# Kernel tuning notes

Hardware: AMD Instinct MI355X
Metric: run time of the kernel (lower is better)

## Reference

```python
import jax, jax.numpy as jnp
import numpy as np

B, S, H, NH, HD = 2, 2048, 4096, 32, 128
THETA = 10000.0


def rotate_half(x):
    x1, x2 = jnp.split(x, 2, axis=-1)
    return jnp.concatenate((-x2, x1), axis=-1)


def setup_inputs() -> dict:
    key = jax.random.key(0)
    ks = jax.random.split(key, 6)
    hidden_states = jax.random.normal(ks[0], (B, S, H), dtype=jnp.float32)
    # additive causal mask, [1,1,S,S]
    causal = jnp.triu(jnp.full((S, S), -1e9, dtype=jnp.float32), k=1)
    attention_mask = causal[None, None, :, :]
    scale = 0.02
    Wq = jax.random.normal(ks[1], (H, H), dtype=jnp.float32) * scale
    Wk = jax.random.normal(ks[2], (H, H), dtype=jnp.float32) * scale
    Wv = jax.random.normal(ks[3], (H, H), dtype=jnp.float32) * scale
    Wo = jax.random.normal(ks[4], (H, H), dtype=jnp.float32) * scale
    return {"hidden_states": hidden_states, "attention_mask": attention_mask,
            "Wq": Wq, "Wk": Wk, "Wv": Wv, "Wo": Wo}


def _rope_tables(seq_len, dtype):
    inv_freq = 1.0 / (THETA ** (jnp.arange(0, HD, 2, dtype=jnp.float32) / HD))
    t = jnp.arange(seq_len, dtype=jnp.float32)
    freqs = jnp.einsum('i,j->ij', t, inv_freq)          # [S, HD/2]
    emb = jnp.concatenate((freqs, freqs), axis=-1)       # [S, HD]
    return jnp.cos(emb).astype(dtype), jnp.sin(emb).astype(dtype)


def reference(hidden_states, attention_mask, Wq, Wk, Wv, Wo):
    b, s, _ = hidden_states.shape
    # nn.Linear: y = x @ W.T
    q = jnp.einsum('bsh,oh->bso', hidden_states, Wq).reshape(b, s, NH, HD).transpose(0, 2, 1, 3)
    k = jnp.einsum('bsh,oh->bso', hidden_states, Wk).reshape(b, s, NH, HD).transpose(0, 2, 1, 3)
    v = jnp.einsum('bsh,oh->bso', hidden_states, Wv).reshape(b, s, NH, HD).transpose(0, 2, 1, 3)
    cos, sin = _rope_tables(s, q.dtype)                  # [S, HD] broadcast over b,h
    q = q * cos + rotate_half(q) * sin
    k = k * cos + rotate_half(k) * sin
    scores = jnp.einsum('bhqd,bhkd->bhqk', q, k) / jnp.sqrt(jnp.asarray(HD, q.dtype))
    scores = scores + attention_mask
    attn = jax.nn.softmax(scores.astype(jnp.float32), axis=-1).astype(q.dtype)
    out = jnp.einsum('bhqk,bhkd->bhqd', attn, v)
    out = out.transpose(0, 2, 1, 3).reshape(b, s, H)
    return jnp.einsum('bsh,oh->bso', out, Wo)
```

## Files before the change

### kernel.cpp

```cpp
#include <hip/hip_runtime.h>
#include <stdint.h>

typedef __attribute__((ext_vector_type(4))) float f32x4;
typedef __attribute__((ext_vector_type(8))) short bf16x8;
typedef __attribute__((ext_vector_type(4))) unsigned int u32x4;

__device__ __forceinline__ short f2bf(float x) {
  unsigned int u = __builtin_bit_cast(unsigned int, x);
  unsigned int r = (u + 0x7fffu + ((u >> 16) & 1u)) >> 16;
  return (short)r;
}
__device__ __forceinline__ float bf2f(short s) {
  unsigned int u = ((unsigned int)(unsigned short)s) << 16;
  return __builtin_bit_cast(float, u);
}
__device__ __forceinline__ unsigned pkbf(float lo, float hi) {
  unsigned r;
  asm("v_cvt_pk_bf16_f32 %0, %1, %2" : "=v"(r) : "v"(lo), "v"(hi));
  return r;
}

__device__ __forceinline__ void gload_lds16(const void* g, void* l) {
  __builtin_amdgcn_global_load_lds(
      (const __attribute__((address_space(1))) void*)g,
      (__attribute__((address_space(3))) void*)l, 16, 0, 0);
}

__global__ __launch_bounds__(256) void cvt_bf16(const float* __restrict__ in,
                                                short* __restrict__ out, int n) {
  int idx = blockIdx.x * blockDim.x + threadIdx.x;
  int stride = gridDim.x * blockDim.x;
  for (int i = idx * 4; i < n; i += stride * 4) {
    float4 v = *(const float4*)(in + i);
    short4 o;
    o.x = f2bf(v.x); o.y = f2bf(v.y); o.z = f2bf(v.z); o.w = f2bf(v.w);
    *(short4*)(out + i) = o;
  }
}

__global__ __launch_bounds__(256) void rope_table_k(float2* __restrict__ tab) {
  int idx = blockIdx.x * 256 + threadIdx.x;
  int s = idx >> 6, j = idx & 63;
  float invf = powf(10000.0f, -((float)j) / 64.0f);
  float a = (float)s * invf;
  tab[idx] = make_float2(cosf(a), sinf(a));
}

__global__ __launch_bounds__(256) void rope_apply_k(short* __restrict__ Qb,
                                                    short* __restrict__ Kb,
                                                    const float2* __restrict__ tab) {
  bool isK = (blockIdx.y != 0);
  short* base = isK ? Kb : Qb;
  float post = isK ? 1.0f : (0.08838834764831845f * 1.4426950408889634f);
  int token = blockIdx.x;
  int s = token & 2047;
  short* rowp = base + (size_t)token * 4096;
  const float2* trow = tab + s * 64;
  for (int u = threadIdx.x; u < 512; u += 256) {
    int h = u >> 4;
    int d0 = (u & 15) * 4;
    short* p1 = rowp + h * 128 + d0;
    short* p2 = p1 + 64;
    short4 a = *(short4*)p1, b = *(short4*)p2;
    short4 ra, rb;
#pragma unroll
    for (int j = 0; j < 4; ++j) {
      short aj = (&a.x)[j], bj = (&b.x)[j];
      float qa = bf2f(aj), qb = bf2f(bj);
      float2 cs = trow[d0 + j];
      (&ra.x)[j] = f2bf((qa * cs.x - qb * cs.y) * post);
      (&rb.x)[j] = f2bf((qb * cs.x + qa * cs.y) * post);
    }
    *(short4*)p1 = ra;
    *(short4*)p2 = rb;
  }
}

template <int MODE>
__global__ __launch_bounds__(512) void gemm256(const short* __restrict__ A,
                                               const short* __restrict__ Bw,
                                               void* __restrict__ out) {
  __shared__ __attribute__((aligned(16))) short smem[3 * 16384];
  int wg = blockIdx.x;
  int xcd = wg & 7, i = wg >> 3;
  int by = xcd * 2 + (i >> 4);
  int bx = i & 15;
  int tid = threadIdx.x;
  int w = tid >> 6, lane = tid & 63;
  int l16 = lane & 15, l4 = lane >> 4;
  int wm = w >> 2, wn = w & 3;

  f32x4 acc[8][4] = {};

  const short* Ab = A + (size_t)(by * 256) * 4096;
  const short* Bb = Bw + (size_t)(bx * 256) * 4096;
  int idx0 = tid, idx1 = 512 + tid;
  int r0 = idx0 >> 2, c0l = (idx0 & 3) ^ (r0 & 3);
  int r1 = idx1 >> 2, c1l = (idx1 & 3) ^ (r1 & 3);
  int db0 = (0 * 512 + w * 64) * 8;
  int db1 = (1 * 512 + w * 64) * 8;

  auto STAGE = [&](int kt, int ob) {
    gload_lds16(Ab + (size_t)r0 * 4096 + kt * 32 + c0l * 8, &smem[ob + db0]);
    gload_lds16(Ab + (size_t)r1 * 4096 + kt * 32 + c1l * 8, &smem[ob + db1]);
    gload_lds16(Bb + (size_t)r0 * 4096 + kt * 32 + c0l * 8, &smem[ob + 8192 + db0]);
    gload_lds16(Bb + (size_t)r1 * 4096 + kt * 32 + c1l * 8, &smem[ob + 8192 + db1]);
  };

  int o0 = 0, o1 = 16384, o2 = 32768;
  STAGE(0, o0);
  STAGE(1, o1);

  const int physc = l4 ^ (l16 & 3);
  const int arow = wm * 128 + l16;
  const int brow = wn * 64 + l16;

  auto COMPUTE = [&](int ob) {
    const short* lA = &smem[ob];
    const short* lB = &smem[ob + 8192];
    bf16x8 af[4], bfr[4];
#pragma unroll
    for (int nf = 0; nf < 4; ++nf)
      bfr[nf] = *(const bf16x8*)&lB[(brow + nf * 16) * 32 + physc * 8];
#pragma unroll
    for (int mf = 0; mf < 4; ++mf)
      af[mf] = *(const bf16x8*)&lA[(arow + mf * 16) * 32 + physc * 8];
    __builtin_amdgcn_s_setprio(1);
#pragma unroll
    for (int mf = 0; mf < 4; ++mf)
#pragma unroll
      for (int nf = 0; nf < 4; ++nf)
        acc[mf][nf] = __builtin_amdgcn_mfma_f32_16x16x32_bf16(af[mf], bfr[nf], acc[mf][nf], 0, 0, 0);
    __builtin_amdgcn_s_setprio(0);
#pragma unroll
    for (int mf = 0; mf < 4; ++mf)
      af[mf] = *(const bf16x8*)&lA[(arow + 64 + mf * 16) * 32 + physc * 8];
    __builtin_amdgcn_s_setprio(1);
#pragma unroll
    for (int mf = 0; mf < 4; ++mf)
#pragma unroll
      for (int nf = 0; nf < 4; ++nf)
        acc[mf + 4][nf] = __builtin_amdgcn_mfma_f32_16x16x32_bf16(af[mf], bfr[nf], acc[mf + 4][nf], 0, 0, 0);
    __builtin_amdgcn_s_setprio(0);
  };

  for (int t = 0; t < 127; ++t) {
    asm volatile("s_waitcnt vmcnt(4)" ::: "memory");
    __builtin_amdgcn_s_barrier();
    asm volatile("" ::: "memory");
    if (t + 2 < 128) STAGE(t + 2, o2);
    COMPUTE(o0);
    int tmp = o0; o0 = o1; o1 = o2; o2 = tmp;
  }
  asm volatile("s_waitcnt vmcnt(0)" ::: "memory");
  __builtin_amdgcn_s_barrier();
  asm volatile("" ::: "memory");
  COMPUTE(o0);

  int orow0 = by * 256 + wm * 128;
  int ocol0 = bx * 256 + wn * 64;
#pragma unroll
  for (int mf = 0; mf < 8; ++mf)
#pragma unroll
    for (int nf = 0; nf < 4; ++nf)
#pragma unroll
      for (int ii = 0; ii < 4; ++ii) {
        int r = orow0 + mf * 16 + l4 * 4 + ii;
        int c = ocol0 + nf * 16 + l16;
        float v = acc[mf][nf][ii];
        if constexpr (MODE == 0) {
          ((short*)out)[(size_t)r * 4096 + c] = f2bf(v);
        } else if constexpr (MODE == 1) {
          ((float*)out)[(size_t)r * 4096 + c] = v;
        } else {
          int bb = r >> 11, ss = r & 2047;
          int h = c >> 7, d = c & 127;
          ((short*)out)[(((size_t)((bb * 32 + h) * 128 + d)) << 11) + ss] = f2bf(v);
        }
      }
}

__global__ __launch_bounds__(256) void attn_k(const short* __restrict__ Qb,
                                              const short* __restrict__ Kb,
                                              const short* __restrict__ Vt,
                                              short* __restrict__ AO) {
  __shared__ __attribute__((aligned(16))) short smem[2 * 16384];
  int p = blockIdx.x;
  int bh = p & 63;
  int qt = 15 - (p >> 6);
  int b = bh >> 5, h = bh & 31;
  int tid = threadIdx.x, w = tid >> 6, lane = tid & 63;
  int l16 = lane & 15, l4 = lane >> 4;

  const int nt = 2 * qt + 2;
  const int qbase = qt * 128 + w * 32;

  bf16x8 qf[2][4];
  {
    const short* Qg = Qb + (size_t)(b * 2048 + qbase + l16) * 4096 + h * 128 + l4 * 8;
#pragma unroll
    for (int mg = 0; mg < 2; ++mg)
#pragma unroll
      for (int kk = 0; kk < 4; ++kk)
        qf[mg][kk] = *(const bf16x8*)(Qg + (size_t)mg * 16 * 4096 + kk * 32);
  }

  f32x4 oacc[2][8] = {};
  float mrun[2] = {-1e30f, -1e30f}, lsum[2] = {0.f, 0.f};

  const short* Kbase = Kb + (size_t)(b * 2048) * 4096 + h * 128;
  const short* Vbase = Vt + (size_t)bh * 128 * 2048;

  const int srowK = l4, skbK = l16;
  const int srowV = lane >> 3, skbV = lane & 7;

  auto STAGE = [&](int t, int sel) {
    short* lK = &smem[sel * 16384];
    short* lV = lK + 8192;
#pragma unroll
    for (int ii = 0; ii < 4; ++ii) {
      int s = w * 4 + ii;
      int rowK = s * 4 + srowK;
      int srcK = skbK ^ (rowK & 15);
      gload_lds16(Kbase + (size_t)(t * 64 + rowK) * 4096 + srcK * 8, &lK[s * 512]);
      int rowV = s * 8 + srowV;
      int srcV = skbV ^ (rowV & 7);
      gload_lds16(Vbase + (size_t)rowV * 2048 + t * 64 + srcV * 8, &lV[s * 512]);
    }
  };

  STAGE(0, 0);
  __syncthreads();

  const int src0 = l16 | ((2 * (l4 & 1)) << 4);
  const int src1 = src0 | 16;
  const bool hiA = (l4 >> 1) != 0;

  for (int t = 0; t < nt; ++t) {
    int sel = t & 1;
    if (t + 1 < nt) STAGE(t + 1, sel ^ 1);
    const short* lK = &smem[sel * 16384];
    const short* lV = lK + 8192;

    bool full_skip = (t == nt - 1) && (w < 2);
    if (!full_skip) {
      f32x4 sacc[2][4] = {};
#pragma unroll
      for (int kk = 0; kk < 4; ++kk) {
#pragma unroll
        for (int n4 = 0; n4 < 4; ++n4) {
          int row = n4 * 16 + l16;
          int phys = (kk * 4 + l4) ^ (row & 15);
          bf16x8 kf = *(const bf16x8*)&lK[row * 128 + phys * 8];
          sacc[0][n4] = __builtin_amdgcn_mfma_f32_16x16x32_bf16(kf, qf[0][kk], sacc[0][n4], 0, 0, 0);
          sacc[1][n4] = __builtin_amdgcn_mfma_f32_16x16x32_bf16(kf, qf[1][kk], sacc[1][n4], 0, 0, 0);
        }
      }

      if (t >= nt - 2) {
#pragma unroll
        for (int mg = 0; mg < 2; ++mg) {
          int q = qbase + mg * 16 + l16;
#pragma unroll
          for (int n4 = 0; n4 < 4; ++n4)
#pragma unroll
            for (int i = 0; i < 4; ++i) {
              int kv = t * 64 + n4 * 16 + l4 * 4 + i;
              if (kv > q) sacc[mg][n4][i] = -1e30f;
            }
        }
      }

#pragma unroll
      for (int mg = 0; mg < 2; ++mg) {
        float v0 = fmaxf(fmaxf(sacc[mg][0][0], sacc[mg][0][1]), fmaxf(sacc[mg][0][2], sacc[mg][0][3]));
        float v1 = fmaxf(fmaxf(sacc[mg][1][0], sacc[mg][1][1]), fmaxf(sacc[mg][1][2], sacc[mg][1][3]));
        float v2 = fmaxf(fmaxf(sacc[mg][2][0], sacc[mg][2][1]), fmaxf(sacc[mg][2][2], sacc[mg][2][3]));
        float v3 = fmaxf(fmaxf(sacc[mg][3][0], sacc[mg][3][1]), fmaxf(sacc[mg][3][2], sacc[mg][3][3]));
        float vm = fmaxf(fmaxf(v0, v1), fmaxf(v2, v3));
        vm = fmaxf(vm, __shfl_xor(vm, 16));
        vm = fmaxf(vm, __shfl_xor(vm, 32));
        float mn = mrun[mg];
        if (!__all(vm - mn <= 8.0f)) {
          float mnew = fmaxf(mn, vm);
          float fsc = __builtin_amdgcn_exp2f(mn - mnew);
          mrun[mg] = mnew;
          lsum[mg] *= fsc;
#pragma unroll
          for (int dg = 0; dg < 8; ++dg) oacc[mg][dg] *= fsc;
          mn = mnew;
        }
        float psum = 0.f;
#pragma unroll
        for (int n4 = 0; n4 < 4; ++n4)
#pragma unroll
          for (int i = 0; i < 4; ++i) {
            float e = __builtin_amdgcn_exp2f(sacc[mg][n4][i] - mn);
            sacc[mg][n4][i] = e;
            psum += e;
          }
        psum += __shfl_xor(psum, 16);
        psum += __shfl_xor(psum, 32);
        lsum[mg] += psum;
      }

      bf16x8 pb[2][2];
#pragma unroll
      for (int mg = 0; mg < 2; ++mg)
#pragma unroll
        for (int c = 0; c < 2; ++c) {
          unsigned pk0h0 = pkbf(sacc[mg][2 * c][0], sacc[mg][2 * c][1]);
          unsigned pk0h1 = pkbf(sacc[mg][2 * c][2], sacc[mg][2 * c][3]);
          unsigned pk1h0 = pkbf(sacc[mg][2 * c + 1][0], sacc[mg][2 * c + 1][1]);
          unsigned pk1h1 = pkbf(sacc[mg][2 * c + 1][2], sacc[mg][2 * c + 1][3]);
          unsigned s00 = __shfl((int)pk0h0, src0), s10 = __shfl((int)pk1h0, src0);
          unsigned s01 = __shfl((int)pk0h1, src0), s11 = __shfl((int)pk1h1, src0);
          unsigned t00 = __shfl((int)pk0h0, src1), t10 = __shfl((int)pk1h0, src1);
          unsigned t01 = __shfl((int)pk0h1, src1), t11 = __shfl((int)pk1h1, src1);
          u32x4 uw;
          uw[0] = hiA ? s10 : s00;
          uw[1] = hiA ? s11 : s01;
          uw[2] = hiA ? t10 : t00;
          uw[3] = hiA ? t11 : t01;
          pb[mg][c] = __builtin_bit_cast(bf16x8, uw);
        }

#pragma unroll
      for (int c = 0; c < 2; ++c)
#pragma unroll
        for (int dg = 0; dg < 8; ++dg) {
          int d = dg * 16 + l16;
          int phys = (c * 4 + l4) ^ (d & 7);
          bf16x8 vf = *(const bf16x8*)&lV[d * 64 + phys * 8];
          oacc[0][dg] = __builtin_amdgcn_mfma_f32_16x16x32_bf16(vf, pb[0][c], oacc[0][dg], 0, 0, 0);
          oacc[1][dg] = __builtin_amdgcn_mfma_f32_16x16x32_bf16(vf, pb[1][c], oacc[1][dg], 0, 0, 0);
        }
    }
    __syncthreads();
  }

  short* reg = &smem[w * 4096];
  float rls0 = 1.0f / lsum[0], rls1 = 1.0f / lsum[1];
#pragma unroll
  for (int mg = 0; mg < 2; ++mg) {
    float rls = mg ? rls1 : rls0;
    int qloc = mg * 16 + l16;
#pragma unroll
    for (int dg = 0; dg < 8; ++dg) {
      unsigned u0 = pkbf(oacc[mg][dg][0] * rls, oacc[mg][dg][1] * rls);
      unsigned u1 = pkbf(oacc[mg][dg][2] * rls, oacc[mg][dg][3] * rls);
      int c16 = dg * 2 + (l4 >> 1);
      int phys = c16 ^ (qloc & 7);
      int sidx = qloc * 128 + phys * 8 + (l4 & 1) * 4;
      *(uint2*)&reg[sidx] = make_uint2(u0, u1);
    }
  }
#pragma unroll
  for (int pass = 0; pass < 8; ++pass) {
    int qloc = pass * 4 + l4;
    int phys = l16 ^ (qloc & 7);
    bf16x8 v = *(const bf16x8*)&reg[qloc * 128 + phys * 8];
    int qg = qt * 128 + w * 32 + qloc;
    *(bf16x8*)(AO + (size_t)(b * 2048 + qg) * 4096 + h * 128 + l16 * 8) = v;
  }
}

extern "C" void kernel_launch(void* const* d_in, const int* in_sizes, int n_in,
                              void* d_out, int out_size, void* d_ws, size_t ws_size,
                              hipStream_t stream) {
  const float* X = (const float*)d_in[0];
  const float* Wq = (const float*)d_in[2];
  const float* Wk = (const float*)d_in[3];
  const float* Wv = (const float*)d_in[4];
  const float* Wo = (const float*)d_in[5];

  char* ws = (char*)d_ws;
  const size_t SEG = 32ull << 20;
  short* Xb  = (short*)(ws + 0 * SEG);
  short* Wqb = (short*)(ws + 1 * SEG);
  short* Wkb = (short*)(ws + 2 * SEG);
  short* Wvb = (short*)(ws + 3 * SEG);
  short* Qb  = (short*)(ws + 4 * SEG);
  short* Kb  = (short*)(ws + 5 * SEG);
  float2* tab = (float2*)(ws + 6 * SEG);

  const int NE = 4096 * 4096;
  cvt_bf16<<<2048, 256, 0, stream>>>(X, Xb, NE);
  cvt_bf16<<<2048, 256, 0, stream>>>(Wq, Wqb, NE);
  cvt_bf16<<<2048, 256, 0, stream>>>(Wk, Wkb, NE);
  cvt_bf16<<<2048, 256, 0, stream>>>(Wv, Wvb, NE);
  rope_table_k<<<512, 256, 0, stream>>>(tab);

  gemm256<0><<<256, 512, 0, stream>>>(Xb, Wqb, Qb);
  gemm256<0><<<256, 512, 0, stream>>>(Xb, Wkb, Kb);
  short* Vtb = Wqb;
  gemm256<2><<<256, 512, 0, stream>>>(Xb, Wvb, Vtb);

  rope_apply_k<<<dim3(4096, 2), 256, 0, stream>>>(Qb, Kb, tab);

  short* AO = Xb;
  attn_k<<<1024, 256, 0, stream>>>(Qb, Kb, Vtb, AO);

  short* Wob = Wkb;
  cvt_bf16<<<2048, 256, 0, stream>>>(Wo, Wob, NE);
  gemm256<1><<<256, 512, 0, stream>>>(AO, Wob, (float*)d_out);
}
```

Measured before the change: 751.4 us.

## Read V from global memory, halve attention LDS, merge casts into one launch

The attention kernel no longer stages V tiles in LDS. Each wave reads V fragments straight from global memory, which halves shared memory per block, and the kernel requests three blocks per CU through launch bounds. The skip and mask conditions now depend on each wave's own query range, so waves can skip whole tiles lying fully above their causal boundary. The four separate fp32-to-bf16 conversion launches become one launch with a 2D grid. The trade-off is uncoalesced, unshared V loads from global and L2 in place of LDS reuse across waves, in exchange for higher occupancy.

```diff
diff --git a/kernel.cpp b/kernel.cpp
--- a/kernel.cpp
+++ b/kernel.cpp
@@ -24,6 +24,26 @@
   __builtin_amdgcn_global_load_lds(
       (const __attribute__((address_space(1))) void*)g,
       (__attribute__((address_space(3))) void*)l, 16, 0, 0);
+}
+
+__global__ __launch_bounds__(256) void cvt4(const float* __restrict__ a,
+                                            const float* __restrict__ b,
+                                            const float* __restrict__ c,
+                                            const float* __restrict__ d,
+                                            short* __restrict__ oa,
+                                            short* __restrict__ ob,
+                                            short* __restrict__ oc,
+                                            short* __restrict__ od, int n) {
+  const float* in = (blockIdx.y == 0) ? a : (blockIdx.y == 1) ? b : (blockIdx.y == 2) ? c : d;
+  short* out = (blockIdx.y == 0) ? oa : (blockIdx.y == 1) ? ob : (blockIdx.y == 2) ? oc : od;
+  int idx = blockIdx.x * blockDim.x + threadIdx.x;
+  int stride = gridDim.x * blockDim.x;
+  for (int i = idx * 4; i < n; i += stride * 4) {
+    float4 v = *(const float4*)(in + i);
+    short4 o;
+    o.x = f2bf(v.x); o.y = f2bf(v.y); o.z = f2bf(v.z); o.w = f2bf(v.w);
+    *(short4*)(out + i) = o;
+  }
 }
 
 __global__ __launch_bounds__(256) void cvt_bf16(const float* __restrict__ in,
@@ -180,11 +200,11 @@
       }
 }
 
-__global__ __launch_bounds__(256) void attn_k(const short* __restrict__ Qb,
-                                              const short* __restrict__ Kb,
-                                              const short* __restrict__ Vt,
-                                              short* __restrict__ AO) {
-  __shared__ __attribute__((aligned(16))) short smem[2 * 16384];
+__global__ __launch_bounds__(256, 3) void attn_k(const short* __restrict__ Qb,
+                                                 const short* __restrict__ Kb,
+                                                 const short* __restrict__ Vt,
+                                                 short* __restrict__ AO) {
+  __shared__ __attribute__((aligned(16))) short smem[2 * 8192];
   int p = blockIdx.x;
   int bh = p & 63;
   int qt = 15 - (p >> 6);
@@ -212,20 +232,15 @@
   const short* Vbase = Vt + (size_t)bh * 128 * 2048;
 
   const int srowK = l4, skbK = l16;
-  const int srowV = lane >> 3, skbV = lane & 7;
 
   auto STAGE = [&](int t, int sel) {
-    short* lK = &smem[sel * 16384];
-    short* lV = lK + 8192;
+    short* lK = &smem[sel * 8192];
 #pragma unroll
     for (int ii = 0; ii < 4; ++ii) {
       int s = w * 4 + ii;
       int rowK = s * 4 + srowK;
       int srcK = skbK ^ (rowK & 15);
       gload_lds16(Kbase + (size_t)(t * 64 + rowK) * 4096 + srcK * 8, &lK[s * 512]);
-      int rowV = s * 8 + srowV;
-      int srcV = skbV ^ (rowV & 7);
-      gload_lds16(Vbase + (size_t)rowV * 2048 + t * 64 + srcV * 8, &lV[s * 512]);
     }
   };
 
@@ -239,11 +254,10 @@
   for (int t = 0; t < nt; ++t) {
     int sel = t & 1;
     if (t + 1 < nt) STAGE(t + 1, sel ^ 1);
-    const short* lK = &smem[sel * 16384];
-    const short* lV = lK + 8192;
-
-    bool full_skip = (t == nt - 1) && (w < 2);
-    if (!full_skip) {
+    const short* lK = &smem[sel * 8192];
+
+    bool skip = (t * 64 > qbase + 31);
+    if (!skip) {
       f32x4 sacc[2][4] = {};
 #pragma unroll
       for (int kk = 0; kk < 4; ++kk) {
@@ -257,7 +271,7 @@
         }
       }
 
-      if (t >= nt - 2) {
+      if (t * 64 + 63 > qbase) {
 #pragma unroll
         for (int mg = 0; mg < 2; ++mg) {
           int q = qbase + mg * 16 + l16;
@@ -326,15 +340,15 @@
         }
 
 #pragma unroll
-      for (int c = 0; c < 2; ++c)
+      for (int c = 0; c < 2; ++c) {
+        const short* Vg = Vbase + t * 64 + c * 32 + l4 * 8;
 #pragma unroll
         for (int dg = 0; dg < 8; ++dg) {
-          int d = dg * 16 + l16;
-          int phys = (c * 4 + l4) ^ (d & 7);
-          bf16x8 vf = *(const bf16x8*)&lV[d * 64 + phys * 8];
+          bf16x8 vf = *(const bf16x8*)(Vg + (size_t)(dg * 16 + l16) * 2048);
           oacc[0][dg] = __builtin_amdgcn_mfma_f32_16x16x32_bf16(vf, pb[0][c], oacc[0][dg], 0, 0, 0);
           oacc[1][dg] = __builtin_amdgcn_mfma_f32_16x16x32_bf16(vf, pb[1][c], oacc[1][dg], 0, 0, 0);
         }
+      }
     }
     __syncthreads();
   }
@@ -385,10 +399,7 @@
   float2* tab = (float2*)(ws + 6 * SEG);
 
   const int NE = 4096 * 4096;
-  cvt_bf16<<<2048, 256, 0, stream>>>(X, Xb, NE);
-  cvt_bf16<<<2048, 256, 0, stream>>>(Wq, Wqb, NE);
-  cvt_bf16<<<2048, 256, 0, stream>>>(Wk, Wkb, NE);
-  cvt_bf16<<<2048, 256, 0, stream>>>(Wv, Wvb, NE);
+  cvt4<<<dim3(2048, 4), 256, 0, stream>>>(X, Wq, Wk, Wv, Xb, Wqb, Wkb, Wvb, NE);
   rope_table_k<<<512, 256, 0, stream>>>(tab);
 
   gemm256<0><<<256, 512, 0, stream>>>(Xb, Wqb, Qb);
```

Measured after the change: 843.1 us. 12.2% more time.
